# Optimization experiments

Hardware: AMD Instinct MI355X
Metric: run time of the kernel (lower is better)

Reference implementation:

```python
import jax, jax.numpy as jnp
import numpy as np

B, N, F, E = 256, 784, 1, 6272   # batch, nodes, in-features, edges
C = 32                            # GraphConv channels
H = 512                           # fc1 hidden units
N_OUT = 10


def setup_inputs() -> dict:
    key = jax.random.key(0)
    ks = jax.random.split(key, 12)
    x = jax.random.normal(ks[0], (B, N, F), dtype=jnp.float32)
    edge_row = jax.random.randint(ks[1], (E,), 0, N, dtype=jnp.int32)
    edge_col = jax.random.randint(ks[2], (E,), 0, N, dtype=jnp.int32)
    edge_val = jax.random.uniform(ks[3], (E,), dtype=jnp.float32)
    # GraphConv weights (Glorot-ish scale)
    W1 = jax.random.normal(ks[4], (F, C), dtype=jnp.float32) * 0.5
    b1 = jnp.zeros((C,), dtype=jnp.float32)
    W2 = jax.random.normal(ks[5], (C, C), dtype=jnp.float32) * 0.18
    b2 = jnp.zeros((C,), dtype=jnp.float32)
    # MLP head
    Wf1 = jax.random.normal(ks[6], (N * C, H), dtype=jnp.float32) * 0.01
    bf1 = jnp.zeros((H,), dtype=jnp.float32)
    Wf2 = jax.random.normal(ks[7], (H, N_OUT), dtype=jnp.float32) * 0.04
    bf2 = jnp.zeros((N_OUT,), dtype=jnp.float32)
    return {"x": x, "edge_row": edge_row, "edge_col": edge_col, "edge_val": edge_val,
            "W1": W1, "b1": b1, "W2": W2, "b2": b2,
            "Wf1": Wf1, "bf1": bf1, "Wf2": Wf2, "bf2": bf2}


def _spmm(h, row, col, val):
    # h: [B, N, C]; sparse fltr (COO) @ h per batch element
    msg = jnp.swapaxes(h[:, col, :], 0, 1) * val[:, None, None]      # [E, B, C]
    agg = jax.ops.segment_sum(msg, row, num_segments=N)              # [N, B, C]
    return jnp.swapaxes(agg, 0, 1)                                   # [B, N, C]


def reference(x, edge_row, edge_col, edge_val, W1, b1, W2, b2, Wf1, bf1, Wf2, bf2):
    # GraphConv 1: elu(fltr @ x @ W1 + b1)
    h = jax.nn.elu(_spmm(x, edge_row, edge_col, edge_val) @ W1 + b1)
    # GraphConv 2
    h = jax.nn.elu(_spmm(h, edge_row, edge_col, edge_val) @ W2 + b2)
    # Flatten -> Dense(512, relu) -> Dense(10, softmax)
    flat = h.reshape(B, N * C)
    z = jax.nn.relu(flat @ Wf1 + bf1)
    return jax.nn.softmax(z @ Wf2 + bf2, axis=-1)
```

## Files before the change

kernel.cpp:

```cpp
#include <hip/hip_runtime.h>
#include <hip/hip_bf16.h>

#define B_ 256
#define N_ 784
#define E_ 6272
#define C_ 32
#define H_ 512
#define NK 25088
#define BC 8192
#define S_SPLIT 28
#define KHALF 12544

typedef __attribute__((ext_vector_type(8))) short short8;
typedef __attribute__((ext_vector_type(4))) float f32x4;

__device__ __forceinline__ float elu1(float v) {
  return v > 0.f ? v : (__expf(v) - 1.f);
}

__device__ __forceinline__ unsigned short bf16b(float v) {
  __hip_bfloat16 h = __float2bfloat16(v);
  return *reinterpret_cast<unsigned short*>(&h);
}

__device__ __forceinline__ unsigned int pk2(float lo, float hi) {
  return (unsigned int)bf16b(lo) | ((unsigned int)bf16b(hi) << 16);
}

__device__ __forceinline__ void acc2(unsigned u, float val, float& a0, float& a1) {
  float lo = __uint_as_float(u << 16);
  float hi = __uint_as_float(u & 0xffff0000u);
  a0 = fmaf(val, lo, a0);
  a1 = fmaf(val, hi, a1);
}

__global__ __launch_bounds__(1024) void k_prep(
    const int* __restrict__ erow, const int* __restrict__ ecol,
    const float* __restrict__ eval, const float* __restrict__ x,
    int* __restrict__ row_ptr, int* __restrict__ col_s, float* __restrict__ val_s,
    float* __restrict__ xT) {
  const int t = threadIdx.x;
  if (blockIdx.x == 0) {
    __shared__ int cnt[N_];
    __shared__ int off[N_];
    __shared__ int bufA[1024];
    __shared__ int bufB[1024];
    if (t < N_) cnt[t] = 0;
    __syncthreads();
    for (int e = t; e < E_; e += 1024) atomicAdd(&cnt[erow[e]], 1);
    __syncthreads();
    bufA[t] = (t < N_) ? cnt[t] : 0;
    __syncthreads();
    int* src = bufA; int* dst = bufB;
    for (int d = 1; d < 1024; d <<= 1) {
      int v = src[t];
      if (t >= d) v += src[t - d];
      dst[t] = v;
      __syncthreads();
      int* tmp = src; src = dst; dst = tmp;
    }
    if (t < N_) {
      int ex = src[t] - cnt[t];
      off[t] = ex;
      row_ptr[t] = ex;
    }
    if (t == 0) row_ptr[N_] = E_;
    __syncthreads();
    for (int e = t; e < E_; e += 1024) {
      int r = erow[e];
      int p = atomicAdd(&off[r], 1);
      col_s[p] = ecol[e];
      val_s[p] = eval[e];
    }
  } else {
    __shared__ float tile[32][33];
    int bid = blockIdx.x - 1;
    int n0 = (bid % 25) * 32, b0 = (bid / 25) * 32;
    int ni = t & 31, bi = t >> 5;
    int n = n0 + ni;
    if (n < N_) tile[ni][bi] = x[(b0 + bi) * N_ + n];
    __syncthreads();
    int nj = t >> 5, bj = t & 31;
    int nw = n0 + nj;
    if (nw < N_) xT[nw * B_ + b0 + bj] = tile[nj][bj];
  }
}

__global__ __launch_bounds__(256) void k_gc1(
    const float* __restrict__ xT, const int* __restrict__ row_ptr,
    const int* __restrict__ col_s, const float* __restrict__ val_s,
    const float* __restrict__ W1, const float* __restrict__ b1,
    const float* __restrict__ Wf1, __hip_bfloat16* __restrict__ wf1t,
    __hip_bfloat16* __restrict__ h1) {
  __shared__ union {
    struct { int lc[64]; float lv[64]; } g;
    float tile[64][65];
  } sm;
  int t = threadIdx.x;
  if (blockIdx.x < N_) {
    int n = blockIdx.x;
    int e0 = row_ptr[n], deg = row_ptr[n + 1] - e0;
    float agg = 0.f;
    for (int base = 0; base < deg; base += 64) {
      int m = min(64, deg - base);
      __syncthreads();
      if (t < m) { sm.g.lc[t] = col_s[e0 + base + t]; sm.g.lv[t] = val_s[e0 + base + t]; }
      __syncthreads();
      int e = 0;
      for (; e + 4 <= m; e += 4) {
        float x0 = xT[sm.g.lc[e + 0] * B_ + t];
        float x1 = xT[sm.g.lc[e + 1] * B_ + t];
        float x2 = xT[sm.g.lc[e + 2] * B_ + t];
        float x3 = xT[sm.g.lc[e + 3] * B_ + t];
        agg = fmaf(sm.g.lv[e + 0], x0, agg);
        agg = fmaf(sm.g.lv[e + 1], x1, agg);
        agg = fmaf(sm.g.lv[e + 2], x2, agg);
        agg = fmaf(sm.g.lv[e + 3], x3, agg);
      }
      for (; e < m; ++e)
        agg = fmaf(sm.g.lv[e], xT[sm.g.lc[e] * B_ + t], agg);
    }
    union { unsigned int u[16]; uint4 v[4]; } ob;
#pragma unroll
    for (int c = 0; c < C_; c += 2) {
      float o0 = elu1(fmaf(agg, W1[c], b1[c]));
      float o1 = elu1(fmaf(agg, W1[c + 1], b1[c + 1]));
      ob.u[c >> 1] = pk2(o0, o1);
    }
    uint4* dst = reinterpret_cast<uint4*>(h1 + (size_t)n * BC + t * C_);
#pragma unroll
    for (int j = 0; j < 4; ++j) dst[j] = ob.v[j];
  } else {
    int bid = blockIdx.x - N_;
    int k0 = (bid % 196) * 64, n0 = (bid / 196) * 64;
#pragma unroll
    for (int it = 0; it < 16; ++it) {
      int idx = it * 256 + t;
      int kk = idx >> 6, nn = idx & 63;
      sm.tile[kk][nn] = Wf1[(size_t)(k0 + kk) * H_ + n0 + nn];
    }
    __syncthreads();
#pragma unroll
    for (int it = 0; it < 8; ++it) {
      int idx = it * 256 + t;
      int nn = idx >> 5, kp = idx & 31;
      unsigned int v = pk2(sm.tile[2 * kp][nn], sm.tile[2 * kp + 1][nn]);
      *reinterpret_cast<unsigned int*>(
          wf1t + (size_t)(n0 + nn) * NK + k0 + 2 * kp) = v;
    }
  }
}

__global__ __launch_bounds__(64) void k_gc2(
    const __hip_bfloat16* __restrict__ h1, const int* __restrict__ row_ptr,
    const int* __restrict__ col_s, const float* __restrict__ val_s,
    const float* __restrict__ W2, const float* __restrict__ b2,
    const float* __restrict__ Wf1, __hip_bfloat16* __restrict__ wf1t,
    __hip_bfloat16* __restrict__ flat) {
  __shared__ union {
    struct { int lc[64]; float lv[64]; } g;
    float tile[32][33];
  } sm;
  int bid = blockIdx.x;
  int t = threadIdx.x;
  if (bid < N_ * 4) {
    int q = bid & 3;
    int n = bid >> 2;
    int tb = q * 64 + t;
    int e0 = row_ptr[n], deg = row_ptr[n + 1] - e0;
    float acc[C_];
#pragma unroll
    for (int c = 0; c < C_; ++c) acc[c] = 0.f;

#define ACC16(v0, v1, v2, v3, val) do {                                       \
    acc2(v0.x, val, acc[0], acc[1]);  acc2(v0.y, val, acc[2], acc[3]);        \
    acc2(v0.z, val, acc[4], acc[5]);  acc2(v0.w, val, acc[6], acc[7]);        \
    acc2(v1.x, val, acc[8], acc[9]);  acc2(v1.y, val, acc[10], acc[11]);      \
    acc2(v1.z, val, acc[12], acc[13]); acc2(v1.w, val, acc[14], acc[15]);     \
    acc2(v2.x, val, acc[16], acc[17]); acc2(v2.y, val, acc[18], acc[19]);     \
    acc2(v2.z, val, acc[20], acc[21]); acc2(v2.w, val, acc[22], acc[23]);     \
    acc2(v3.x, val, acc[24], acc[25]); acc2(v3.y, val, acc[26], acc[27]);     \
    acc2(v3.z, val, acc[28], acc[29]); acc2(v3.w, val, acc[30], acc[31]);     \
  } while (0)

    for (int base = 0; base < deg; base += 64) {
      int m = min(64, deg - base);
      __syncthreads();
      if (t < m) { sm.g.lc[t] = col_s[e0 + base + t]; sm.g.lv[t] = val_s[e0 + base + t]; }
      __syncthreads();
      int e = 0;
      for (; e + 4 <= m; e += 4) {
        const uint4* p0 = reinterpret_cast<const uint4*>(h1 + (size_t)sm.g.lc[e + 0] * BC + tb * C_);
        const uint4* p1 = reinterpret_cast<const uint4*>(h1 + (size_t)sm.g.lc[e + 1] * BC + tb * C_);
        const uint4* p2 = reinterpret_cast<const uint4*>(h1 + (size_t)sm.g.lc[e + 2] * BC + tb * C_);
        const uint4* p3 = reinterpret_cast<const uint4*>(h1 + (size_t)sm.g.lc[e + 3] * BC + tb * C_);
        uint4 a0 = p0[0], a1 = p0[1], a2 = p0[2], a3 = p0[3];
        uint4 b0 = p1[0], b1 = p1[1], b2v = p1[2], b3 = p1[3];
        uint4 c0 = p2[0], c1 = p2[1], c2 = p2[2], c3 = p2[3];
        uint4 d0 = p3[0], d1 = p3[1], d2 = p3[2], d3 = p3[3];
        float va = sm.g.lv[e], vb = sm.g.lv[e + 1], vc = sm.g.lv[e + 2], vd = sm.g.lv[e + 3];
        ACC16(a0, a1, a2, a3, va);
        ACC16(b0, b1, b2v, b3, vb);
        ACC16(c0, c1, c2, c3, vc);
        ACC16(d0, d1, d2, d3, vd);
      }
      for (; e < m; ++e) {
        const uint4* p0 = reinterpret_cast<const uint4*>(h1 + (size_t)sm.g.lc[e] * BC + tb * C_);
        uint4 a0 = p0[0], a1 = p0[1], a2 = p0[2], a3 = p0[3];
        ACC16(a0, a1, a2, a3, sm.g.lv[e]);
      }
    }
#undef ACC16

    union { unsigned int u[16]; uint4 v[4]; } ob;
#pragma unroll
    for (int c2 = 0; c2 < C_; c2 += 2) {
      float o0 = b2[c2], o1 = b2[c2 + 1];
#pragma unroll
      for (int c = 0; c < C_; ++c) {
        o0 = fmaf(acc[c], W2[c * C_ + c2], o0);
        o1 = fmaf(acc[c], W2[c * C_ + c2 + 1], o1);
      }
      ob.u[c2 >> 1] = pk2(elu1(o0), elu1(o1));
    }
    uint4* dst = reinterpret_cast<uint4*>(flat + (size_t)tb * NK + n * C_);
#pragma unroll
    for (int j = 0; j < 4; ++j) dst[j] = ob.v[j];
  } else {
    int bid2 = bid - N_ * 4;
    int k0 = KHALF + (bid2 % 392) * 32, n0 = (bid2 / 392) * 32;
#pragma unroll
    for (int it = 0; it < 16; ++it) {
      int idx = it * 64 + t;
      int kk = idx >> 5, nn = idx & 31;
      sm.tile[kk][nn] = Wf1[(size_t)(k0 + kk) * H_ + n0 + nn];
    }
    __syncthreads();
#pragma unroll
    for (int it = 0; it < 8; ++it) {
      int idx = it * 64 + t;
      int nn = idx >> 4, kp = idx & 15;
      unsigned int v = pk2(sm.tile[2 * kp][nn], sm.tile[2 * kp + 1][nn]);
      *reinterpret_cast<unsigned int*>(
          wf1t + (size_t)(n0 + nn) * NK + k0 + 2 * kp) = v;
    }
  }
}

__global__ __launch_bounds__(256, 2) void k_fc1(
    const __hip_bfloat16* __restrict__ flat, const __hip_bfloat16* __restrict__ wf1t,
    float* __restrict__ partial) {
  __shared__ unsigned char lds[3 * 24576];
  int raw = blockIdx.x;
  int bid = (raw & 7) * 56 + (raw >> 3);
  int s = bid >> 4, r16 = bid & 15;
  int m0 = (r16 & 1) * 128;
  int n0 = (r16 >> 1) * 64;
  int k0 = s * 896;
  int tid = threadIdx.x;
  int w = tid >> 6, l = tid & 63;
  int r = l & 15, g = l >> 4;

  const __hip_bfloat16* src[6];
  int ldsoff[6];
#pragma unroll
  for (int j = 0; j < 6; ++j) {
    int reg = w * 6 + j;
    ldsoff[j] = reg * 1024 + l * 16;
    if (reg < 16) {
      int fmg = reg >> 1, ks = reg & 1;
      src[j] = flat + (size_t)(m0 + fmg * 16 + r) * NK + (k0 + ks * 32 + g * 8);
    } else {
      int fng = (reg - 16) >> 1, ks = reg & 1;
      src[j] = wf1t + (size_t)(n0 + fng * 16 + r) * NK + (k0 + ks * 32 + g * 8);
    }
  }

  f32x4 acc[4][2];
#pragma unroll
  for (int i = 0; i < 4; ++i)
#pragma unroll
    for (int j = 0; j < 2; ++j) acc[i][j] = (f32x4){0.f, 0.f, 0.f, 0.f};

#define GLOAD_LDS(gp, lp)                                                     \
  __builtin_amdgcn_global_load_lds(                                           \
      (const __attribute__((address_space(1))) unsigned int*)(gp),            \
      (__attribute__((address_space(3))) unsigned int*)(lp), 16, 0, 0)
#define STAGE(t, buf) do {                                                    \
    _Pragma("unroll")                                                         \
    for (int j = 0; j < 6; ++j)                                               \
      GLOAD_LDS(src[j] + (t) * 64, &lds[(buf) * 24576 + ldsoff[j]]);          \
  } while (0)
#define VWAIT(n) do {                                                         \
    asm volatile("s_waitcnt vmcnt(%0)" :: "n"(n) : "memory");                 \
    __builtin_amdgcn_sched_barrier(0);                                        \
  } while (0)
#define BAR() do {                                                            \
    __builtin_amdgcn_s_barrier();                                             \
    __builtin_amdgcn_sched_barrier(0);                                        \
  } while (0)
#define COMPUTE(buf) do {                                                     \
    const unsigned char* bb = &lds[(buf) * 24576];                            \
    short8 af[4][2], bf[2][2];                                                \
    _Pragma("unroll")                                                         \
    for (int fm = 0; fm < 4; ++fm)                                            \
      _Pragma("unroll")                                                       \
      for (int ks = 0; ks < 2; ++ks)                                          \
        af[fm][ks] = *reinterpret_cast<const short8*>(                        \
            bb + (((4 * (w & 1) + fm) * 2 + ks) << 10) + l * 16);             \
    _Pragma("unroll")                                                         \
    for (int fn = 0; fn < 2; ++fn)                                            \
      _Pragma("unroll")                                                       \
      for (int ks = 0; ks < 2; ++ks)                                          \
        bf[fn][ks] = *reinterpret_cast<const short8*>(                        \
            bb + ((16 + (2 * (w >> 1) + fn) * 2 + ks) << 10) + l * 16);       \
    _Pragma("unroll")                                                         \
    for (int ks = 0; ks < 2; ++ks)                                            \
      _Pragma("unroll")                                                       \
      for (int fn = 0; fn < 2; ++fn)                                          \
        _Pragma("unroll")                                                     \
        for (int fm = 0; fm < 4; ++fm)                                        \
          acc[fm][fn] = __builtin_amdgcn_mfma_f32_16x16x32_bf16(              \
              af[fm][ks], bf[fn][ks], acc[fm][fn], 0, 0, 0);                  \
  } while (0)
#define STEP(t) do {                                                          \
    VWAIT((t) < 13 ? 6 : 0);                                                  \
    BAR();                                                                    \
    if ((t) + 2 <= 13) STAGE((t) + 2, ((t) + 2) % 3);                         \
    COMPUTE((t) % 3);                                                         \
  } while (0)

  STAGE(0, 0);
  STAGE(1, 1);
  STEP(0);  STEP(1);  STEP(2);  STEP(3);  STEP(4);  STEP(5);  STEP(6);
  STEP(7);  STEP(8);  STEP(9);  STEP(10); STEP(11); STEP(12); STEP(13);

#undef GLOAD_LDS
#undef STAGE
#undef VWAIT
#undef BAR
#undef COMPUTE
#undef STEP

  int wm = (w & 1) * 64, wn = (w >> 1) * 32;
  float* p = partial + (size_t)s * (256 * 512);
#pragma unroll
  for (int fm = 0; fm < 4; ++fm)
#pragma unroll
    for (int fn = 0; fn < 2; ++fn)
#pragma unroll
      for (int q = 0; q < 4; ++q) {
        int m = m0 + wm + fm * 16 + g * 4 + q;
        int n = n0 + wn + fn * 16 + r;
        p[m * 512 + n] = acc[fm][fn][q];
      }
}

__global__ __launch_bounds__(512) void k_head(
    const float* __restrict__ partial, const float* __restrict__ bf1,
    const float* __restrict__ Wf2, const float* __restrict__ bf2,
    float* __restrict__ out) {
  __shared__ float red[8][12];
  int b = blockIdx.x;
  int t = threadIdx.x;
  float v = bf1[t];
#pragma unroll
  for (int s = 0; s < S_SPLIT; ++s)
    v += partial[(size_t)s * (256 * 512) + b * 512 + t];
  v = fmaxf(v, 0.f);
  float pacc[10];
#pragma unroll
  for (int j = 0; j < 10; ++j) pacc[j] = v * Wf2[t * 10 + j];
#pragma unroll
  for (int j = 0; j < 10; ++j)
#pragma unroll
    for (int d = 32; d > 0; d >>= 1)
      pacc[j] += __shfl_down(pacc[j], d);
  int wv = t >> 6, ln = t & 63;
  if (ln == 0) {
#pragma unroll
    for (int j = 0; j < 10; ++j) red[wv][j] = pacc[j];
  }
  __syncthreads();
  if (t == 0) {
    float lg[10];
    float m = -1e30f;
#pragma unroll
    for (int j = 0; j < 10; ++j) {
      float z = bf2[j];
#pragma unroll
      for (int wq = 0; wq < 8; ++wq) z += red[wq][j];
      lg[j] = z;
      m = fmaxf(m, z);
    }
    float sum = 0.f;
#pragma unroll
    for (int j = 0; j < 10; ++j) { lg[j] = __expf(lg[j] - m); sum += lg[j]; }
    float inv = 1.f / sum;
#pragma unroll
    for (int j = 0; j < 10; ++j) out[b * 10 + j] = lg[j] * inv;
  }
}

extern "C" void kernel_launch(void* const* d_in, const int* in_sizes, int n_in,
                              void* d_out, int out_size, void* d_ws, size_t ws_size,
                              hipStream_t stream) {
  const float* x    = (const float*)d_in[0];
  const int*   erow = (const int*)d_in[1];
  const int*   ecol = (const int*)d_in[2];
  const float* ev   = (const float*)d_in[3];
  const float* W1   = (const float*)d_in[4];
  const float* b1   = (const float*)d_in[5];
  const float* W2   = (const float*)d_in[6];
  const float* b2   = (const float*)d_in[7];
  const float* Wf1  = (const float*)d_in[8];
  const float* bf1  = (const float*)d_in[9];
  const float* Wf2  = (const float*)d_in[10];
  const float* bf2  = (const float*)d_in[11];
  float* out = (float*)d_out;

  const size_t partial_bytes = (size_t)S_SPLIT * 256 * 512 * 4;
  const size_t flat_bytes    = (size_t)B_ * NK * 2;
  const size_t wf1t_bytes    = (size_t)H_ * NK * 2;

  char* ws = (char*)d_ws;
  float* partial = (float*)ws;
  float* xT = (float*)ws;
  __hip_bfloat16* h1 = (__hip_bfloat16*)(ws + 802816);
  __hip_bfloat16* flat = (__hip_bfloat16*)(ws + partial_bytes);
  __hip_bfloat16* wf1t = (__hip_bfloat16*)(ws + partial_bytes + flat_bytes);
  char* tail = ws + partial_bytes + flat_bytes + wf1t_bytes;
  int*   row_ptr = (int*)tail;
  int*   col_s   = (int*)(tail + 3152);
  float* val_s   = (float*)(tail + 3152 + E_ * 4);

  hipLaunchKernelGGL(k_prep, dim3(1 + 200), dim3(1024), 0, stream,
                     erow, ecol, ev, x, row_ptr, col_s, val_s, xT);
  hipLaunchKernelGGL(k_gc1, dim3(N_ + 196 * 8), dim3(256), 0, stream,
                     xT, row_ptr, col_s, val_s, W1, b1, Wf1, wf1t, h1);
  hipLaunchKernelGGL(k_gc2, dim3(N_ * 4 + 392 * 16), dim3(64), 0, stream,
                     h1, row_ptr, col_s, val_s, W2, b2, Wf1, wf1t, flat);
  hipLaunchKernelGGL(k_fc1, dim3(S_SPLIT * 16), dim3(256), 0, stream,
                     flat, wf1t, partial);
  hipLaunchKernelGGL(k_head, dim3(B_), dim3(512), 0, stream,
                     partial, bf1, Wf2, bf2, out);
}
```

Baseline: 90.28 us.

## Store scalar GC1 aggregate and recompute ELU features inside GC2 gather

GC1 now writes only the scalar aggregated value per node and batch (fp32) instead of materialising the 32-channel bf16 h1 tensor. GC2 gathers that scalar per edge and recomputes elu(s*W1+b1) on the fly for all 32 channels before accumulating. This trades a 32x smaller gather footprint and no h1 write for 32 exp evaluations per edge per thread, and it drops the bf16 rounding of h1.

Result: faster. 85.59 us (-5.2%).

```diff
diff --git a/kernel.cpp b/kernel.cpp
--- a/kernel.cpp
+++ b/kernel.cpp
@@ -7,9 +7,7 @@
 #define C_ 32
 #define H_ 512
 #define NK 25088
-#define BC 8192
 #define S_SPLIT 28
-#define KHALF 12544
 
 typedef __attribute__((ext_vector_type(8))) short short8;
 typedef __attribute__((ext_vector_type(4))) float f32x4;
@@ -25,13 +23,6 @@
 
 __device__ __forceinline__ unsigned int pk2(float lo, float hi) {
   return (unsigned int)bf16b(lo) | ((unsigned int)bf16b(hi) << 16);
-}
-
-__device__ __forceinline__ void acc2(unsigned u, float val, float& a0, float& a1) {
-  float lo = __uint_as_float(u << 16);
-  float hi = __uint_as_float(u & 0xffff0000u);
-  a0 = fmaf(val, lo, a0);
-  a1 = fmaf(val, hi, a1);
 }
 
 __global__ __launch_bounds__(1024) void k_prep(
@@ -89,9 +80,8 @@
 __global__ __launch_bounds__(256) void k_gc1(
     const float* __restrict__ xT, const int* __restrict__ row_ptr,
     const int* __restrict__ col_s, const float* __restrict__ val_s,
-    const float* __restrict__ W1, const float* __restrict__ b1,
     const float* __restrict__ Wf1, __hip_bfloat16* __restrict__ wf1t,
-    __hip_bfloat16* __restrict__ h1) {
+    float* __restrict__ agg1) {
   __shared__ union {
     struct { int lc[64]; float lv[64]; } g;
     float tile[64][65];
@@ -120,16 +110,7 @@
       for (; e < m; ++e)
         agg = fmaf(sm.g.lv[e], xT[sm.g.lc[e] * B_ + t], agg);
     }
-    union { unsigned int u[16]; uint4 v[4]; } ob;
-#pragma unroll
-    for (int c = 0; c < C_; c += 2) {
-      float o0 = elu1(fmaf(agg, W1[c], b1[c]));
-      float o1 = elu1(fmaf(agg, W1[c + 1], b1[c + 1]));
-      ob.u[c >> 1] = pk2(o0, o1);
-    }
-    uint4* dst = reinterpret_cast<uint4*>(h1 + (size_t)n * BC + t * C_);
-#pragma unroll
-    for (int j = 0; j < 4; ++j) dst[j] = ob.v[j];
+    agg1[n * B_ + t] = agg;
   } else {
     int bid = blockIdx.x - N_;
     int k0 = (bid % 196) * 64, n0 = (bid / 196) * 64;
@@ -152,8 +133,9 @@
 }
 
 __global__ __launch_bounds__(64) void k_gc2(
-    const __hip_bfloat16* __restrict__ h1, const int* __restrict__ row_ptr,
+    const float* __restrict__ agg1, const int* __restrict__ row_ptr,
     const int* __restrict__ col_s, const float* __restrict__ val_s,
+    const float* __restrict__ W1, const float* __restrict__ b1,
     const float* __restrict__ W2, const float* __restrict__ b2,
     const float* __restrict__ Wf1, __hip_bfloat16* __restrict__ wf1t,
     __hip_bfloat16* __restrict__ flat) {
@@ -168,21 +150,12 @@
     int n = bid >> 2;
     int tb = q * 64 + t;
     int e0 = row_ptr[n], deg = row_ptr[n + 1] - e0;
+    float w1r[C_], b1r[C_];
+#pragma unroll
+    for (int c = 0; c < C_; ++c) { w1r[c] = W1[c]; b1r[c] = b1[c]; }
     float acc[C_];
 #pragma unroll
     for (int c = 0; c < C_; ++c) acc[c] = 0.f;
-
-#define ACC16(v0, v1, v2, v3, val) do {                                       \
-    acc2(v0.x, val, acc[0], acc[1]);  acc2(v0.y, val, acc[2], acc[3]);        \
-    acc2(v0.z, val, acc[4], acc[5]);  acc2(v0.w, val, acc[6], acc[7]);        \
-    acc2(v1.x, val, acc[8], acc[9]);  acc2(v1.y, val, acc[10], acc[11]);      \
-    acc2(v1.z, val, acc[12], acc[13]); acc2(v1.w, val, acc[14], acc[15]);     \
-    acc2(v2.x, val, acc[16], acc[17]); acc2(v2.y, val, acc[18], acc[19]);     \
-    acc2(v2.z, val, acc[20], acc[21]); acc2(v2.w, val, acc[22], acc[23]);     \
-    acc2(v3.x, val, acc[24], acc[25]); acc2(v3.y, val, acc[26], acc[27]);     \
-    acc2(v3.z, val, acc[28], acc[29]); acc2(v3.w, val, acc[30], acc[31]);     \
-  } while (0)
-
     for (int base = 0; base < deg; base += 64) {
       int m = min(64, deg - base);
       __syncthreads();
@@ -190,28 +163,28 @@
       __syncthreads();
       int e = 0;
       for (; e + 4 <= m; e += 4) {
-        const uint4* p0 = reinterpret_cast<const uint4*>(h1 + (size_t)sm.g.lc[e + 0] * BC + tb * C_);
-        const uint4* p1 = reinterpret_cast<const uint4*>(h1 + (size_t)sm.g.lc[e + 1] * BC + tb * C_);
-        const uint4* p2 = reinterpret_cast<const uint4*>(h1 + (size_t)sm.g.lc[e + 2] * BC + tb * C_);
-        const uint4* p3 = reinterpret_cast<const uint4*>(h1 + (size_t)sm.g.lc[e + 3] * BC + tb * C_);
-        uint4 a0 = p0[0], a1 = p0[1], a2 = p0[2], a3 = p0[3];
-        uint4 b0 = p1[0], b1 = p1[1], b2v = p1[2], b3 = p1[3];
-        uint4 c0 = p2[0], c1 = p2[1], c2 = p2[2], c3 = p2[3];
-        uint4 d0 = p3[0], d1 = p3[1], d2 = p3[2], d3 = p3[3];
-        float va = sm.g.lv[e], vb = sm.g.lv[e + 1], vc = sm.g.lv[e + 2], vd = sm.g.lv[e + 3];
-        ACC16(a0, a1, a2, a3, va);
-        ACC16(b0, b1, b2v, b3, vb);
-        ACC16(c0, c1, c2, c3, vc);
-        ACC16(d0, d1, d2, d3, vd);
+        float s0 = agg1[sm.g.lc[e + 0] * B_ + tb];
+        float s1 = agg1[sm.g.lc[e + 1] * B_ + tb];
+        float s2 = agg1[sm.g.lc[e + 2] * B_ + tb];
+        float s3 = agg1[sm.g.lc[e + 3] * B_ + tb];
+        float v0 = sm.g.lv[e + 0], v1 = sm.g.lv[e + 1];
+        float v2 = sm.g.lv[e + 2], v3 = sm.g.lv[e + 3];
+#pragma unroll
+        for (int c = 0; c < C_; ++c) {
+          acc[c] = fmaf(v0, elu1(fmaf(s0, w1r[c], b1r[c])), acc[c]);
+          acc[c] = fmaf(v1, elu1(fmaf(s1, w1r[c], b1r[c])), acc[c]);
+          acc[c] = fmaf(v2, elu1(fmaf(s2, w1r[c], b1r[c])), acc[c]);
+          acc[c] = fmaf(v3, elu1(fmaf(s3, w1r[c], b1r[c])), acc[c]);
+        }
       }
       for (; e < m; ++e) {
-        const uint4* p0 = reinterpret_cast<const uint4*>(h1 + (size_t)sm.g.lc[e] * BC + tb * C_);
-        uint4 a0 = p0[0], a1 = p0[1], a2 = p0[2], a3 = p0[3];
-        ACC16(a0, a1, a2, a3, sm.g.lv[e]);
+        float s0 = agg1[sm.g.lc[e] * B_ + tb];
+        float v0 = sm.g.lv[e];
+#pragma unroll
+        for (int c = 0; c < C_; ++c)
+          acc[c] = fmaf(v0, elu1(fmaf(s0, w1r[c], b1r[c])), acc[c]);
       }
     }
-#undef ACC16
-
     union { unsigned int u[16]; uint4 v[4]; } ob;
 #pragma unroll
     for (int c2 = 0; c2 < C_; c2 += 2) {
@@ -228,7 +201,7 @@
     for (int j = 0; j < 4; ++j) dst[j] = ob.v[j];
   } else {
     int bid2 = bid - N_ * 4;
-    int k0 = KHALF + (bid2 % 392) * 32, n0 = (bid2 / 392) * 32;
+    int k0 = 12544 + (bid2 % 392) * 32, n0 = (bid2 / 392) * 32;
 #pragma unroll
     for (int it = 0; it < 16; ++it) {
       int idx = it * 64 + t;
@@ -425,8 +398,8 @@
 
   char* ws = (char*)d_ws;
   float* partial = (float*)ws;
-  float* xT = (float*)ws;
-  __hip_bfloat16* h1 = (__hip_bfloat16*)(ws + 802816);
+  float* xT   = (float*)ws;
+  float* agg1 = (float*)(ws + 802816);
   __hip_bfloat16* flat = (__hip_bfloat16*)(ws + partial_bytes);
   __hip_bfloat16* wf1t = (__hip_bfloat16*)(ws + partial_bytes + flat_bytes);
   char* tail = ws + partial_bytes + flat_bytes + wf1t_bytes;
@@ -437,9 +410,9 @@
   hipLaunchKernelGGL(k_prep, dim3(1 + 200), dim3(1024), 0, stream,
                      erow, ecol, ev, x, row_ptr, col_s, val_s, xT);
   hipLaunchKernelGGL(k_gc1, dim3(N_ + 196 * 8), dim3(256), 0, stream,
-                     xT, row_ptr, col_s, val_s, W1, b1, Wf1, wf1t, h1);
+                     xT, row_ptr, col_s, val_s, Wf1, wf1t, agg1);
   hipLaunchKernelGGL(k_gc2, dim3(N_ * 4 + 392 * 16), dim3(64), 0, stream,
-                     h1, row_ptr, col_s, val_s, W2, b2, Wf1, wf1t, flat);
+                     agg1, row_ptr, col_s, val_s, W1, b1, W2, b2, Wf1, wf1t, flat);
   hipLaunchKernelGGL(k_fc1, dim3(S_SPLIT * 16), dim3(256), 0, stream,
                      flat, wf1t, partial);
   hipLaunchKernelGGL(k_head, dim3(B_), dim3(512), 0, stream,
```
